# Kernel optimization log

Hardware: AMD Instinct MI355X
Metric: run time of the kernel (lower is better)

The kernel has to match this reference:

```python
import jax, jax.numpy as jnp
import numpy as np

H = 2048        # hidden size
NH = 16         # query heads
NKV = 8         # kv heads
HD = 128        # head dim
I = 8192        # intermediate size
EPS = 1e-6
SPLITS = [4194304, 6291456, 8388608, 12582912, 29360128, 46137344]
TOTAL = 62914560


def setup_inputs() -> dict:
    key = jax.random.key(0)
    k1, k2 = jax.random.split(key)
    B, S = 1, 2048
    hidden_states = jax.random.normal(k1, (B, S, H), dtype=jnp.float32)
    flat_weights = jax.random.normal(k2, (TOTAL,), dtype=jnp.float32) * 0.02
    input_ln_w = jnp.ones((H,), dtype=jnp.float32)
    post_ln_w = jnp.ones((H,), dtype=jnp.float32)
    # RoPE tables (Llama theta=10000)
    inv_freq = 1.0 / (10000.0 ** (np.arange(0, HD, 2, dtype=np.float32) / HD))
    ang = np.arange(S, dtype=np.float32)[:, None] * inv_freq[None, :]   # [S, HD/2]
    emb = np.concatenate([ang, ang], axis=-1)                            # [S, HD]
    cos = jnp.asarray(np.cos(emb), dtype=jnp.float32)
    sin = jnp.asarray(np.sin(emb), dtype=jnp.float32)
    return {"hidden_states": hidden_states, "flat_weights": flat_weights,
            "input_ln_w": input_ln_w, "post_ln_w": post_ln_w, "cos": cos, "sin": sin}


def _rms_norm(x, w):
    var = jnp.mean(x * x, axis=-1, keepdims=True)
    return w * (x * jax.lax.rsqrt(var + EPS))


def _rotate_half(x):
    x1, x2 = jnp.split(x, 2, axis=-1)
    return jnp.concatenate([-x2, x1], axis=-1)


def _apply_rope(q, k, cos, sin):
    # q: [B,NH,S,HD], k: [B,NKV,S,HD]; cos/sin: [S,HD]
    c = cos[None, None, :, :]
    s = sin[None, None, :, :]
    return q * c + _rotate_half(q) * s, k * c + _rotate_half(k) * s


def _decoder_layer(hidden_states, flat_weights, input_ln_w, post_ln_w, cos, sin):
    # Simulates dfloat11_decode output: split flat reconstructed weights
    # (split order in source: q, k, v, o, up, gate, down)
    parts = jnp.split(flat_weights, SPLITS)
    q_w = parts[0].reshape(NH * HD, H)
    k_w = parts[1].reshape(NKV * HD, H)
    v_w = parts[2].reshape(NKV * HD, H)
    o_w = parts[3].reshape(H, NH * HD)
    up_w = parts[4].reshape(I, H)
    gate_w = parts[5].reshape(I, H)
    down_w = parts[6].reshape(H, I)

    B, S, _ = hidden_states.shape
    residual = hidden_states
    x = _rms_norm(hidden_states, input_ln_w)

    q = (x @ q_w.T).reshape(B, S, NH, HD).transpose(0, 2, 1, 3)    # [B,NH,S,HD]
    k = (x @ k_w.T).reshape(B, S, NKV, HD).transpose(0, 2, 1, 3)   # [B,NKV,S,HD]
    v = (x @ v_w.T).reshape(B, S, NKV, HD).transpose(0, 2, 1, 3)
    q, k = _apply_rope(q, k, cos, sin)

    # GQA: repeat kv heads
    rep = NH // NKV
    k = jnp.repeat(k, rep, axis=1)   # [B,NH,S,HD]
    v = jnp.repeat(v, rep, axis=1)

    scores = jnp.einsum("bhqd,bhkd->bhqk", q, k) / jnp.sqrt(jnp.float32(HD))
    causal = jnp.tril(jnp.ones((S, S), dtype=bool))
    scores = jnp.where(causal[None, None], scores, jnp.finfo(scores.dtype).min)
    probs = jax.nn.softmax(scores, axis=-1)
    attn = jnp.einsum("bhqk,bhkd->bhqd", probs, v)                  # [B,NH,S,HD]
    attn = attn.transpose(0, 2, 1, 3).reshape(B, S, NH * HD)
    hidden = residual + attn @ o_w.T

    residual = hidden
    x = _rms_norm(hidden, post_ln_w)
    mlp = (jax.nn.silu(x @ gate_w.T) * (x @ up_w.T)) @ down_w.T
    return residual + mlp


def reference(hidden_states, flat_weights, input_ln_w, post_ln_w, cos, sin):
    return _decoder_layer(hidden_states, flat_weights, input_ln_w, post_ln_w, cos, sin)
```

## Files before the change

kernel.cpp:

```cpp
#include <hip/hip_runtime.h>
#include <type_traits>
#include <cstdint>
#include <cstddef>

typedef __bf16 bf16x8 __attribute__((ext_vector_type(8)));
typedef float  f32x4  __attribute__((ext_vector_type(4)));
typedef unsigned short u16v4 __attribute__((ext_vector_type(4)));
typedef unsigned short u16v8 __attribute__((ext_vector_type(8)));

#define H    2048
#define NH   16
#define NKV  8
#define HD   128
#define II   8192
#define S    2048

__device__ __forceinline__ unsigned short f2bf(float f) {
    union { float f; unsigned u; } v; v.f = f;
    unsigned r = v.u + 0x7fffu + ((v.u >> 16) & 1u);
    return (unsigned short)(r >> 16);
}
__device__ __forceinline__ float bf2f(unsigned short b) {
    union { unsigned u; float f; } v; v.u = ((unsigned)b) << 16;
    return v.f;
}

__device__ __forceinline__ void async16(const unsigned short* g, const unsigned short* l) {
    __builtin_amdgcn_global_load_lds(
        (const __attribute__((address_space(1))) void*)g,
        (__attribute__((address_space(3))) void*)l, 16, 0, 0);
}

__global__ __launch_bounds__(256) void w2bf(const float* __restrict__ src,
                                            unsigned short* __restrict__ dst)
{
    const size_t i = (size_t)blockIdx.x * 256 + threadIdx.x;
    float4 a = ((const float4*)src)[2 * i];
    float4 b = ((const float4*)src)[2 * i + 1];
    u16v8 o;
    o[0] = f2bf(a.x); o[1] = f2bf(a.y); o[2] = f2bf(a.z); o[3] = f2bf(a.w);
    o[4] = f2bf(b.x); o[5] = f2bf(b.y); o[6] = f2bf(b.z); o[7] = f2bf(b.w);
    ((u16v8*)dst)[i] = o;
}

__global__ __launch_bounds__(256) void w2bf_mlp(const float* __restrict__ src,
                                                unsigned short* __restrict__ dst)
{
    const int p = blockIdx.x;
    const int g = p >> 7, r = p & 127;
    const int half = r >> 6;
    const int c = (g << 6) + (r & 63);
    const float* s = src + ((size_t)half * II + c) * H;
    unsigned short* d = dst + (size_t)p * H;
    const int t = threadIdx.x;
    float4 a = ((const float4*)s)[2 * t];
    float4 b = ((const float4*)s)[2 * t + 1];
    u16v8 o;
    o[0] = f2bf(a.x); o[1] = f2bf(a.y); o[2] = f2bf(a.z); o[3] = f2bf(a.w);
    o[4] = f2bf(b.x); o[5] = f2bf(b.y); o[6] = f2bf(b.z); o[7] = f2bf(b.w);
    *(u16v8*)&d[t * 8] = o;
}

__global__ __launch_bounds__(256) void rmsnorm_kernel(
    const float* __restrict__ x, const float* __restrict__ w,
    unsigned short* __restrict__ out)
{
    __shared__ float red[4];
    const int row = blockIdx.x;
    const int tid = threadIdx.x;
    const float* xr = x + (size_t)row * H;
    float4 v0 = ((const float4*)xr)[tid];
    float4 v1 = ((const float4*)xr)[256 + tid];
    float s = v0.x*v0.x + v0.y*v0.y + v0.z*v0.z + v0.w*v0.w
            + v1.x*v1.x + v1.y*v1.y + v1.z*v1.z + v1.w*v1.w;
    #pragma unroll
    for (int o = 1; o < 64; o <<= 1) s += __shfl_xor(s, o);
    if ((tid & 63) == 0) red[tid >> 6] = s;
    __syncthreads();
    float tot = red[0] + red[1] + red[2] + red[3];
    float rinv = rsqrtf(tot * (1.0f / (float)H) + 1e-6f);
    float4 w0 = ((const float4*)w)[tid];
    float4 w1 = ((const float4*)w)[256 + tid];
    u16v4 o0, o1;
    o0[0] = f2bf(v0.x * w0.x * rinv); o0[1] = f2bf(v0.y * w0.y * rinv);
    o0[2] = f2bf(v0.z * w0.z * rinv); o0[3] = f2bf(v0.w * w0.w * rinv);
    o1[0] = f2bf(v1.x * w1.x * rinv); o1[1] = f2bf(v1.y * w1.y * rinv);
    o1[2] = f2bf(v1.z * w1.z * rinv); o1[3] = f2bf(v1.w * w1.w * rinv);
    unsigned short* orow = out + (size_t)row * H;
    *(u16v4*)&orow[tid * 4]        = o0;
    *(u16v4*)&orow[1024 + tid * 4] = o1;
}

template<typename OutT, bool ATOMIC, bool SILU>
__global__ __launch_bounds__(256) void gemm_bf16(
    const unsigned short* __restrict__ A, const unsigned short* __restrict__ B,
    OutT* __restrict__ C, int M, int N, int K, int lda, int kslice)
{
    __shared__ unsigned short SM[8192];
    unsigned short* As = SM;
    unsigned short* Bs = SM + 4096;
    const int tid  = threadIdx.x;
    const int wave = tid >> 6, lane = tid & 63;
    const int quad = lane >> 4, l16 = lane & 15;
    const int m0 = blockIdx.y * 128, n0 = blockIdx.x * 128;
    const int wm = (wave >> 1) * 64, wn = (wave & 1) * 64;
    const int kbeg = blockIdx.z * kslice;

    const int sr = lane >> 2;
    const int sc = (lane & 3) * 8;
    const unsigned short* Ag0 = A + (size_t)(m0 + wave * 16 + sr) * lda + sc + kbeg;
    const unsigned short* Ag1 = Ag0 + (size_t)64 * lda;
    const unsigned short* Bg0 = B + (size_t)(n0 + wave * 16 + sr) * K + sc + kbeg;
    const unsigned short* Bg1 = Bg0 + (size_t)64 * K;
    const unsigned short* Al0 = &As[(wave * 16) * 32];
    const unsigned short* Al1 = &As[(64 + wave * 16) * 32];
    const unsigned short* Bl0 = &Bs[(wave * 16) * 32];
    const unsigned short* Bl1 = &Bs[(64 + wave * 16) * 32];

    f32x4 acc[4][4] = {};

    for (int k0 = 0; k0 < kslice; k0 += 32) {
        async16(Ag0 + k0, Al0);
        async16(Ag1 + k0, Al1);
        async16(Bg0 + k0, Bl0);
        async16(Bg1 + k0, Bl1);
        __syncthreads();

        bf16x8 af[4], bfm[4];
        #pragma unroll
        for (int i = 0; i < 4; i++)
            af[i] = *(const bf16x8*)&As[(wm + i * 16 + l16) * 32 + quad * 8];
        #pragma unroll
        for (int i = 0; i < 4; i++)
            bfm[i] = *(const bf16x8*)&Bs[(wn + i * 16 + l16) * 32 + quad * 8];
        #pragma unroll
        for (int mi = 0; mi < 4; mi++)
            #pragma unroll
            for (int ni = 0; ni < 4; ni++)
                acc[mi][ni] = __builtin_amdgcn_mfma_f32_16x16x32_bf16(
                    af[mi], bfm[ni], acc[mi][ni], 0, 0, 0);
        __syncthreads();
    }

    if constexpr (SILU) {
        if (wave & 1) {
            #pragma unroll
            for (int mi = 0; mi < 4; mi++)
                #pragma unroll
                for (int r = 0; r < 4; r++) {
                    const int lm = wm + mi * 16 + quad * 4 + r;
                    #pragma unroll
                    for (int ni = 0; ni < 4; ni++)
                        SM[lm * 64 + ni * 16 + l16] = f2bf(acc[mi][ni][r]);
                }
        }
        __syncthreads();
        if (!(wave & 1)) {
            const int colbase = blockIdx.x * 64;
            #pragma unroll
            for (int mi = 0; mi < 4; mi++)
                #pragma unroll
                for (int r = 0; r < 4; r++) {
                    const int lm = wm + mi * 16 + quad * 4 + r;
                    const size_t rowoff = (size_t)(m0 + lm) * N;
                    #pragma unroll
                    for (int ni = 0; ni < 4; ni++) {
                        const int c = ni * 16 + l16;
                        float g = bf2f(SM[lm * 64 + c]);
                        float u = acc[mi][ni][r];
                        float sig = 1.0f / (1.0f + exp2f(-g * 1.4426950408889634f));
                        C[rowoff + colbase + c] = f2bf(g * sig * u);
                    }
                }
        }
        return;
    }

    #pragma unroll
    for (int mi = 0; mi < 4; mi++) {
        #pragma unroll
        for (int r = 0; r < 4; r++) {
            const int m = m0 + wm + mi * 16 + quad * 4 + r;
            const size_t rowoff = (size_t)m * N;
            #pragma unroll
            for (int ni = 0; ni < 4; ni++) {
                const int n = n0 + wn + ni * 16 + l16;
                float v = acc[mi][ni][r];
                if constexpr (ATOMIC) {
                    atomicAdd((float*)&C[rowoff + n], v);
                } else if constexpr (std::is_same<OutT, float>::value) {
                    C[rowoff + n] = v;
                } else {
                    C[rowoff + n] = f2bf(v);
                }
            }
        }
    }
}

__global__ __launch_bounds__(256) void rope_prep(
    const float* __restrict__ qkv, const float* __restrict__ cosp,
    const float* __restrict__ sinp,
    unsigned short* __restrict__ q_r, unsigned short* __restrict__ k_r)
{
    const int s = blockIdx.x;
    const int tid = threadIdx.x;
    const float* row = qkv + (size_t)s * 4096;
    #pragma unroll
    for (int j = 0; j < 12; j++) {
        int e = j * 256 + tid;
        int head = e >> 7, hd = e & 127;
        float v = row[e];
        float part = (hd < 64) ? -row[e + 64] : row[e - 64];
        float c  = cosp[s * HD + hd];
        float sn = sinp[s * HD + hd];
        unsigned short ob = f2bf(v * c + part * sn);
        if (head < NH) q_r[((size_t)head * S + s) * HD + hd] = ob;
        else           k_r[((size_t)(head - NH) * S + s) * HD + hd] = ob;
    }
}

__global__ __launch_bounds__(256) void v_trans(
    const float* __restrict__ qkv, unsigned short* __restrict__ v_t)
{
    __shared__ unsigned short t[128][66];
    const int s0 = blockIdx.x * 64;
    const int kv = blockIdx.y;
    const int tid = threadIdx.x;
    const float* base = qkv + 3072 + kv * HD;
    #pragma unroll
    for (int i = 0; i < 8; i++) {
        int idx4 = i * 256 + tid;
        int s_l = idx4 >> 5;
        int hd4 = (idx4 & 31) * 4;
        float4 v = *(const float4*)(base + (size_t)(s0 + s_l) * 4096 + hd4);
        t[hd4 + 0][s_l] = f2bf(v.x);
        t[hd4 + 1][s_l] = f2bf(v.y);
        t[hd4 + 2][s_l] = f2bf(v.z);
        t[hd4 + 3][s_l] = f2bf(v.w);
    }
    __syncthreads();
    #pragma unroll
    for (int i = 0; i < 8; i++) {
        int idx = i * 256 + tid;
        int d  = idx >> 4;
        int rm = idx & 15;
        int hh = rm >> 3;
        int s4 = (rm & 7) * 4;
        u16v4 o;
        o[0] = t[d][hh * 32 + s4];     o[1] = t[d][hh * 32 + s4 + 1];
        o[2] = t[d][hh * 32 + s4 + 2]; o[3] = t[d][hh * 32 + s4 + 3];
        size_t tile = (size_t)kv * (S / 32) + (s0 >> 5) + hh;
        *(u16v4*)&v_t[(tile * 128 + d) * 32 + s4] = o;
    }
}

__global__ __launch_bounds__(256) void attn_kernel(
    const unsigned short* __restrict__ q_r, const unsigned short* __restrict__ k_r,
    const unsigned short* __restrict__ v_t, unsigned short* __restrict__ out)
{
    __shared__ unsigned short Ks[32 * 128];
    __shared__ unsigned short Vs[144 * 32];
    __shared__ unsigned short P[4][16][40];
    const int h = blockIdx.y, kv = h >> 1;
    const int qb0 = blockIdx.x * 64;
    const int tid = threadIdx.x;
    const int wave = tid >> 6, lane = tid & 63, quad = lane >> 4, l16 = lane & 15;
    const int qb = qb0 + wave * 16;
    const unsigned short* Q  = q_r + (size_t)h * S * HD;
    const unsigned short* K  = k_r + (size_t)kv * S * HD;
    const unsigned short* Vh = v_t + (size_t)kv * (S / 32) * (128 * 32);

    {
        int e0 = tid * 2;
        Vs[128 * 32 + e0]     = (e0     < 32) ? (unsigned short)0x3F80 : (unsigned short)0;
        Vs[128 * 32 + e0 + 1] = (e0 + 1 < 32) ? (unsigned short)0x3F80 : (unsigned short)0;
    }

    bf16x8 aq[4];
    #pragma unroll
    for (int t = 0; t < 4; t++)
        aq[t] = *(const bf16x8*)&Q[(size_t)(qb + l16) * HD + t * 32 + quad * 8];

    f32x4 o[9] = {};
    float m_i[4] = { -__builtin_inff(), -__builtin_inff(), -__builtin_inff(), -__builtin_inff() };
    const float SCL = 0.08838834764831845f * 1.4426950408889634f;
    const int nk = (qb0 >> 5) + 2;

    const int kr  = (lane >> 4);
    const int kbl = lane & 15;
    const int vr  = (lane >> 2);
    const int vbl = lane & 3;

    for (int kb = 0; kb < nk; kb++) {
        const int kbase = kb * 32;
        const unsigned short* Ktile = K + (size_t)kbase * HD;
        const unsigned short* Vtile = Vh + (size_t)kb * (128 * 32);
        #pragma unroll
        for (int e = 0; e < 2; e++) {
            int r = wave * 8 + e * 4 + kr;
            async16(Ktile + r * 128 + ((kbl ^ (r & 15)) * 8), &Ks[(wave * 8 + e * 4) * 128]);
        }
        #pragma unroll
        for (int e = 0; e < 2; e++) {
            int d = wave * 32 + e * 16 + vr;
            async16(Vtile + d * 32 + ((vbl ^ (d & 3)) * 8), &Vs[(wave * 32 + e * 16) * 32]);
        }
        __syncthreads();

        if (kbase <= qb + 15) {
            f32x4 s0 = {0.f, 0.f, 0.f, 0.f}, s1 = {0.f, 0.f, 0.f, 0.f};
            #pragma unroll
            for (int t = 0; t < 4; t++) {
                int b = t * 4 + quad;
                bf16x8 b0 = *(const bf16x8*)&Ks[l16 * 128 + ((b ^ l16) * 8)];
                bf16x8 b1 = *(const bf16x8*)&Ks[(16 + l16) * 128 + ((b ^ l16) * 8)];
                s0 = __builtin_amdgcn_mfma_f32_16x16x32_bf16(aq[t], b0, s0, 0, 0, 0);
                s1 = __builtin_amdgcn_mfma_f32_16x16x32_bf16(aq[t], b1, s1, 0, 0, 0);
            }
            float alpha[4];
            #pragma unroll
            for (int r = 0; r < 4; r++) {
                const int q = qb + quad * 4 + r;
                float v0 = (kbase + l16      <= q) ? s0[r] * SCL : -__builtin_inff();
                float v1 = (kbase + 16 + l16 <= q) ? s1[r] * SCL : -__builtin_inff();
                float mx = fmaxf(v0, v1);
                #pragma unroll
                for (int d = 1; d < 16; d <<= 1) mx = fmaxf(mx, __shfl_xor(mx, d));
                float nm = fmaxf(m_i[r], mx);
                alpha[r] = exp2f(m_i[r] - nm);
                m_i[r] = nm;
                s0[r] = exp2f(v0 - nm);
                s1[r] = exp2f(v1 - nm);
            }
            #pragma unroll
            for (int ni = 0; ni < 9; ni++)
                #pragma unroll
                for (int r = 0; r < 4; r++) o[ni][r] *= alpha[r];
            #pragma unroll
            for (int r = 0; r < 4; r++) {
                P[wave][quad * 4 + r][l16]      = f2bf(s0[r]);
                P[wave][quad * 4 + r][16 + l16] = f2bf(s1[r]);
            }
            asm volatile("s_waitcnt lgkmcnt(0)" ::: "memory");
            bf16x8 ap = *(const bf16x8*)&P[wave][l16][quad * 8];
            #pragma unroll
            for (int ni = 0; ni < 9; ni++) {
                int d = ni * 16 + l16;
                bf16x8 bv = *(const bf16x8*)&Vs[d * 32 + ((quad ^ (d & 3)) * 8)];
                o[ni] = __builtin_amdgcn_mfma_f32_16x16x32_bf16(ap, bv, o[ni], 0, 0, 0);
            }
        }
        __syncthreads();
    }
    #pragma unroll
    for (int r = 0; r < 4; r++) {
        float lsum = __shfl(o[8][r], quad * 16);
        const float inv = 1.0f / lsum;
        const int qrow = qb + quad * 4 + r;
        #pragma unroll
        for (int ni = 0; ni < 8; ni++)
            out[(size_t)qrow * (NH * HD) + h * HD + ni * 16 + l16] = f2bf(o[ni][r] * inv);
    }
}

extern "C" void kernel_launch(void* const* d_in, const int* in_sizes, int n_in,
                              void* d_out, int out_size, void* d_ws, size_t ws_size,
                              hipStream_t stream) {
    const float* hs   = (const float*)d_in[0];
    const float* W    = (const float*)d_in[1];
    const float* ln1  = (const float*)d_in[2];
    const float* ln2  = (const float*)d_in[3];
    const float* cosp = (const float*)d_in[4];
    const float* sinp = (const float*)d_in[5];
    float* out = (float*)d_out;
    char* ws = (char*)d_ws;

    unsigned short* Wbuf   = (unsigned short*)(ws + 0);
    unsigned short* x_norm = (unsigned short*)(ws + (64ull  << 20));
    float*          qkv    = (float*)(ws + (72ull  << 20));
    unsigned short* act    = (unsigned short*)(ws + (72ull  << 20));
    unsigned short* q_r    = (unsigned short*)(ws + (104ull << 20));
    unsigned short* k_r    = (unsigned short*)(ws + (112ull << 20));
    unsigned short* v_t    = (unsigned short*)(ws + (116ull << 20));
    unsigned short* attn_o = (unsigned short*)(ws + (120ull << 20));

    w2bf<<<8388608 / 2048, 256, 0, stream>>>(W, Wbuf);
    rmsnorm_kernel<<<S, 256, 0, stream>>>(hs, ln1, x_norm);
    hipMemsetAsync(qkv, 0, (size_t)S * 4096 * sizeof(float), stream);
    gemm_bf16<float, true, false><<<dim3(4096 / 128, S / 128, 2), 256, 0, stream>>>(
        x_norm, Wbuf, qkv, S, 4096, H, H, H / 2);
    rope_prep<<<S, 256, 0, stream>>>(qkv, cosp, sinp, q_r, k_r);
    v_trans<<<dim3(S / 64, NKV), 256, 0, stream>>>(qkv, v_t);
    attn_kernel<<<dim3(S / 64, NH), 256, 0, stream>>>(q_r, k_r, v_t, attn_o);
    w2bf<<<4194304 / 2048, 256, 0, stream>>>(W + 8388608, Wbuf);
    hipMemcpyAsync(out, hs, (size_t)S * H * sizeof(float), hipMemcpyDeviceToDevice, stream);
    gemm_bf16<float, true, false><<<dim3(H / 128, S / 128, 4), 256, 0, stream>>>(
        attn_o, Wbuf, out, S, H, H, H, H / 4);
    rmsnorm_kernel<<<S, 256, 0, stream>>>(out, ln2, x_norm);
    w2bf_mlp<<<2 * II, 256, 0, stream>>>(W + 12582912, Wbuf);
    gemm_bf16<unsigned short, false, true><<<dim3((2 * II) / 128, S / 128, 1), 256, 0, stream>>>(
        x_norm, Wbuf, act, S, II, H, H, H);
    w2bf<<<16777216 / 2048, 256, 0, stream>>>(W + 46137344, Wbuf);
    gemm_bf16<float, true, false><<<dim3(H / 128, S / 128, 8), 256, 0, stream>>>(
        act, Wbuf, out, S, H, II, II, II / 8);
}
```

Measured before the change: 994.8 us.

## Store QKV in bf16 without split-K, fuse residual into O-proj, swap grid order

The QKV projection now writes a bf16 output directly with no split-K atomics, which removes its fp32 memset and halves the traffic read by rope/v_trans. The residual copy is replaced by adding hs inside the O-projection epilogue, after a zero memset. Split-K factors are reduced for the O and down projections. A SWAP template puts M tiles on blockIdx.x so that consecutive blocks share the same weight tile in cache. The cost is rounding the QKV intermediate to bf16 and fewer blocks in the reduced split-K GEMMs.

```diff
diff --git a/kernel.cpp b/kernel.cpp
--- a/kernel.cpp
+++ b/kernel.cpp
@@ -91,10 +91,11 @@
     *(u16v4*)&orow[1024 + tid * 4] = o1;
 }
 
-template<typename OutT, bool ATOMIC, bool SILU>
+template<typename OutT, bool ATOMIC, bool SILU, bool SWAP>
 __global__ __launch_bounds__(256) void gemm_bf16(
     const unsigned short* __restrict__ A, const unsigned short* __restrict__ B,
-    OutT* __restrict__ C, int M, int N, int K, int lda, int kslice)
+    OutT* __restrict__ C, const float* __restrict__ R,
+    int M, int N, int K, int lda, int kslice)
 {
     __shared__ unsigned short SM[8192];
     unsigned short* As = SM;
@@ -102,7 +103,9 @@
     const int tid  = threadIdx.x;
     const int wave = tid >> 6, lane = tid & 63;
     const int quad = lane >> 4, l16 = lane & 15;
-    const int m0 = blockIdx.y * 128, n0 = blockIdx.x * 128;
+    const int nt = SWAP ? blockIdx.y : blockIdx.x;
+    const int mt = SWAP ? blockIdx.x : blockIdx.y;
+    const int m0 = mt * 128, n0 = nt * 128;
     const int wm = (wave >> 1) * 64, wn = (wave & 1) * 64;
     const int kbeg = blockIdx.z * kslice;
 
@@ -156,7 +159,7 @@
         }
         __syncthreads();
         if (!(wave & 1)) {
-            const int colbase = blockIdx.x * 64;
+            const int colbase = nt * 64;
             #pragma unroll
             for (int mi = 0; mi < 4; mi++)
                 #pragma unroll
@@ -187,6 +190,7 @@
                 const int n = n0 + wn + ni * 16 + l16;
                 float v = acc[mi][ni][r];
                 if constexpr (ATOMIC) {
+                    if (R != nullptr && blockIdx.z == 0) v += R[rowoff + n];
                     atomicAdd((float*)&C[rowoff + n], v);
                 } else if constexpr (std::is_same<OutT, float>::value) {
                     C[rowoff + n] = v;
@@ -199,19 +203,19 @@
 }
 
 __global__ __launch_bounds__(256) void rope_prep(
-    const float* __restrict__ qkv, const float* __restrict__ cosp,
+    const unsigned short* __restrict__ qkv, const float* __restrict__ cosp,
     const float* __restrict__ sinp,
     unsigned short* __restrict__ q_r, unsigned short* __restrict__ k_r)
 {
     const int s = blockIdx.x;
     const int tid = threadIdx.x;
-    const float* row = qkv + (size_t)s * 4096;
+    const unsigned short* row = qkv + (size_t)s * 4096;
     #pragma unroll
     for (int j = 0; j < 12; j++) {
         int e = j * 256 + tid;
         int head = e >> 7, hd = e & 127;
-        float v = row[e];
-        float part = (hd < 64) ? -row[e + 64] : row[e - 64];
+        float v = bf2f(row[e]);
+        float part = (hd < 64) ? -bf2f(row[e + 64]) : bf2f(row[e - 64]);
         float c  = cosp[s * HD + hd];
         float sn = sinp[s * HD + hd];
         unsigned short ob = f2bf(v * c + part * sn);
@@ -221,23 +225,21 @@
 }
 
 __global__ __launch_bounds__(256) void v_trans(
-    const float* __restrict__ qkv, unsigned short* __restrict__ v_t)
+    const unsigned short* __restrict__ qkv, unsigned short* __restrict__ v_t)
 {
     __shared__ unsigned short t[128][66];
     const int s0 = blockIdx.x * 64;
     const int kv = blockIdx.y;
     const int tid = threadIdx.x;
-    const float* base = qkv + 3072 + kv * HD;
-    #pragma unroll
-    for (int i = 0; i < 8; i++) {
-        int idx4 = i * 256 + tid;
-        int s_l = idx4 >> 5;
-        int hd4 = (idx4 & 31) * 4;
-        float4 v = *(const float4*)(base + (size_t)(s0 + s_l) * 4096 + hd4);
-        t[hd4 + 0][s_l] = f2bf(v.x);
-        t[hd4 + 1][s_l] = f2bf(v.y);
-        t[hd4 + 2][s_l] = f2bf(v.z);
-        t[hd4 + 3][s_l] = f2bf(v.w);
+    const unsigned short* base = qkv + 3072 + kv * HD;
+    #pragma unroll
+    for (int i = 0; i < 4; i++) {
+        int idx = i * 256 + tid;
+        int s_l = idx >> 4;
+        int hd8 = (idx & 15) * 8;
+        u16v8 v = *(const u16v8*)(base + (size_t)(s0 + s_l) * 4096 + hd8);
+        #pragma unroll
+        for (int j = 0; j < 8; j++) t[hd8 + j][s_l] = v[j];
     }
     __syncthreads();
     #pragma unroll
@@ -378,7 +380,7 @@
 
     unsigned short* Wbuf   = (unsigned short*)(ws + 0);
     unsigned short* x_norm = (unsigned short*)(ws + (64ull  << 20));
-    float*          qkv    = (float*)(ws + (72ull  << 20));
+    unsigned short* qkv    = (unsigned short*)(ws + (72ull  << 20));
     unsigned short* act    = (unsigned short*)(ws + (72ull  << 20));
     unsigned short* q_r    = (unsigned short*)(ws + (104ull << 20));
     unsigned short* k_r    = (unsigned short*)(ws + (112ull << 20));
@@ -387,21 +389,20 @@
 
     w2bf<<<8388608 / 2048, 256, 0, stream>>>(W, Wbuf);
     rmsnorm_kernel<<<S, 256, 0, stream>>>(hs, ln1, x_norm);
-    hipMemsetAsync(qkv, 0, (size_t)S * 4096 * sizeof(float), stream);
-    gemm_bf16<float, true, false><<<dim3(4096 / 128, S / 128, 2), 256, 0, stream>>>(
-        x_norm, Wbuf, qkv, S, 4096, H, H, H / 2);
+    gemm_bf16<unsigned short, false, false, true><<<dim3(S / 128, 4096 / 128, 1), 256, 0, stream>>>(
+        x_norm, Wbuf, qkv, nullptr, S, 4096, H, H, H);
     rope_prep<<<S, 256, 0, stream>>>(qkv, cosp, sinp, q_r, k_r);
     v_trans<<<dim3(S / 64, NKV), 256, 0, stream>>>(qkv, v_t);
     attn_kernel<<<dim3(S / 64, NH), 256, 0, stream>>>(q_r, k_r, v_t, attn_o);
     w2bf<<<4194304 / 2048, 256, 0, stream>>>(W + 8388608, Wbuf);
-    hipMemcpyAsync(out, hs, (size_t)S * H * sizeof(float), hipMemcpyDeviceToDevice, stream);
-    gemm_bf16<float, true, false><<<dim3(H / 128, S / 128, 4), 256, 0, stream>>>(
-        attn_o, Wbuf, out, S, H, H, H, H / 4);
+    hipMemsetAsync(out, 0, (size_t)S * H * sizeof(float), stream);
+    gemm_bf16<float, true, false, false><<<dim3(H / 128, S / 128, 2), 256, 0, stream>>>(
+        attn_o, Wbuf, out, hs, S, H, H, H, H / 2);
     rmsnorm_kernel<<<S, 256, 0, stream>>>(out, ln2, x_norm);
     w2bf_mlp<<<2 * II, 256, 0, stream>>>(W + 12582912, Wbuf);
-    gemm_bf16<unsigned short, false, true><<<dim3((2 * II) / 128, S / 128, 1), 256, 0, stream>>>(
-        x_norm, Wbuf, act, S, II, H, H, H);
+    gemm_bf16<unsigned short, false, true, true><<<dim3(S / 128, (2 * II) / 128, 1), 256, 0, stream>>>(
+        x_norm, Wbuf, act, nullptr, S, II, H, H, H);
     w2bf<<<16777216 / 2048, 256, 0, stream>>>(W + 46137344, Wbuf);
-    gemm_bf16<float, true, false><<<dim3(H / 128, S / 128, 8), 256, 0, stream>>>(
-        act, Wbuf, out, S, H, II, II, II / 8);
-}
+    gemm_bf16<float, true, false, false><<<dim3(H / 128, S / 128, 4), 256, 0, stream>>>(
+        act, Wbuf, out, nullptr, S, H, II, II, II / 4);
+}
```

Result: faster. 926.5 us (-6.9%).
